# Optimization experiments

Hardware: AMD Instinct MI355X
Metric: run time of the kernel (lower is better)

## Reference

```python
import jax, jax.numpy as jnp
import numpy as np

N_NODES = 50000
N_EDGES = 400000
D = 128


def _rgg_layer(x, src, tgt, Wk, Wq, Wv, Ws, b, n_nodes):
    # Node-level projections (dense GEMMs, as in PyG which applies Linear before message passing)
    k = x @ Wk  # lin_key, gathered at targets
    q = x @ Wq  # lin_query, gathered at sources
    v = x @ Wv  # lin_value, gathered at sources
    # Per-edge gather + sigmoid gate + elementwise message
    eta = jax.nn.sigmoid(k[tgt] + q[src])  # [E, D]
    msg = eta * v[src]                      # [E, D]
    # Scatter-add aggregation to target nodes
    agg = jax.ops.segment_sum(msg, tgt, num_segments=n_nodes)
    # Root/skip connection + bias
    return agg + x @ Ws + b


def setup_inputs() -> dict:
    key = jax.random.key(0)
    ks = jax.random.split(key, 12)
    s = 1.0 / np.sqrt(D)
    x = jax.random.normal(ks[0], (N_NODES, D), dtype=jnp.float32)
    edge_index = jax.random.randint(ks[1], (2, N_EDGES), 0, N_NODES, dtype=jnp.int64)
    W = lambda k: (jax.random.normal(k, (D, D), dtype=jnp.float32) * s)
    return {
        "x": x,
        "edge_index": edge_index,
        "Wk1": W(ks[2]), "Wq1": W(ks[3]), "Wv1": W(ks[4]), "Ws1": W(ks[5]),
        "b1": jnp.zeros((D,), dtype=jnp.float32),
        "Wk2": W(ks[6]), "Wq2": W(ks[7]), "Wv2": W(ks[8]), "Ws2": W(ks[9]),
        "b2": jnp.zeros((D,), dtype=jnp.float32),
    }


def reference(x, edge_index, Wk1, Wq1, Wv1, Ws1, b1, Wk2, Wq2, Wv2, Ws2, b2):
    src, tgt = edge_index[0], edge_index[1]
    n = x.shape[0]
    h = _rgg_layer(x, src, tgt, Wk1, Wq1, Wv1, Ws1, b1, n)
    h = jax.nn.relu(h)
    # F.dropout treated as identity (deterministic/inference reference)
    out = _rgg_layer(h, src, tgt, Wk2, Wq2, Wv2, Ws2, b2, n)
    return out
```

## Files before the change

### kernel.cpp

```cpp
#include <hip/hip_runtime.h>

#define N_NODES 50000
#define D 128
#define N_EDGES 400000
#define NCHUNKS ((N_NODES + 255) / 256)
#define NBLK64 ((N_NODES + 63) / 64)
#define W_FRAG_SHORTS 16384

#define CVT_BLOCKS 3125
#define MW_BLOCKS  64
#define HIST_BLOCKS ((N_EDGES + 255) / 256)
#define PREP_BLOCKS (CVT_BLOCKS + MW_BLOCKS + HIST_BLOCKS)

typedef short s8v  __attribute__((ext_vector_type(8)));
typedef float f4v  __attribute__((ext_vector_type(4)));

__device__ __forceinline__ unsigned int f2bf(float f) {
    unsigned int u = __float_as_uint(f);
    u += 0x7FFFu + ((u >> 16) & 1u);
    return u >> 16;
}
__device__ __forceinline__ unsigned int packbf(float a, float b) {
    return (f2bf(b) << 16) | f2bf(a);
}
__device__ __forceinline__ float bflo(unsigned int u) { return __uint_as_float(u << 16); }
__device__ __forceinline__ float bfhi(unsigned int u) { return __uint_as_float(u & 0xFFFF0000u); }
__device__ __forceinline__ float sigm(float x) {
    return __builtin_amdgcn_rcpf(1.f + __expf(-x));
}

__global__ __launch_bounds__(256)
void prep_all(const float* __restrict__ X, short* __restrict__ Xb,
              const float* __restrict__ W0, const float* __restrict__ W1,
              const float* __restrict__ W2, const float* __restrict__ W3,
              const float* __restrict__ W4, const float* __restrict__ W5,
              const float* __restrict__ W6, const float* __restrict__ W7,
              short* __restrict__ Wt,
              const int* __restrict__ tgt, int* __restrict__ counts)
{
    const int b = blockIdx.x;
    if (b < CVT_BLOCKS) {
        const size_t i = ((size_t)b * 256 + threadIdx.x) * 8;
        float4 a0 = *(const float4*)(X + i);
        float4 a1 = *(const float4*)(X + i + 4);
        s8v v;
        v[0] = (short)f2bf(a0.x); v[1] = (short)f2bf(a0.y);
        v[2] = (short)f2bf(a0.z); v[3] = (short)f2bf(a0.w);
        v[4] = (short)f2bf(a1.x); v[5] = (short)f2bf(a1.y);
        v[6] = (short)f2bf(a1.z); v[7] = (short)f2bf(a1.w);
        *(s8v*)(Xb + i) = v;
    } else if (b < CVT_BLOCKS + MW_BLOCKS) {
        const int bb   = b - CVT_BLOCKS;
        const int wsel = bb >> 3;
        const float* W = (wsel == 0) ? W0 : (wsel == 1) ? W1 : (wsel == 2) ? W2 :
                         (wsel == 3) ? W3 : (wsel == 4) ? W4 : (wsel == 5) ? W5 :
                         (wsel == 6) ? W6 : W7;
        const int slot = (bb & 7) * 256 + threadIdx.x;
        const int frag = slot >> 6;
        const int lane = slot & 63;
        const int n    = (frag >> 2) * 16 + (lane & 15);
        const int kc   = frag & 3;
        const int quad = lane >> 4;
        const int k0   = kc * 32 + quad * 8;
        s8v v;
#pragma unroll
        for (int j = 0; j < 8; ++j)
            v[j] = (short)f2bf(W[(size_t)(k0 + j) * D + n]);
        *(s8v*)(Wt + (size_t)wsel * W_FRAG_SHORTS + (size_t)slot * 8) = v;
    } else {
        const int e = (b - CVT_BLOCKS - MW_BLOCKS) * 256 + threadIdx.x;
        if (e < N_EDGES) atomicAdd(&counts[tgt[e]], 1);
    }
}

__global__ __launch_bounds__(256)
void csr_scan(const int* __restrict__ counts, int* __restrict__ off,
              int* __restrict__ cursor, int* __restrict__ done_ctr,
              int* __restrict__ chunk_sum)
{
    __shared__ int s[256];
    const int b = blockIdx.x, t = threadIdx.x;
    const int i = b * 256 + t;
    const int v = (i < N_NODES) ? counts[i] : 0;
    s[t] = v;
    __syncthreads();
    for (int d = 1; d < 256; d <<= 1) {
        int tt = (t >= d) ? s[t - d] : 0;
        __syncthreads();
        s[t] += tt;
        __syncthreads();
    }
    const int incl = s[t];

    if (t == 255) {
        __hip_atomic_store(&chunk_sum[b], incl, __ATOMIC_RELAXED, __HIP_MEMORY_SCOPE_AGENT);
        __hip_atomic_fetch_add(done_ctr, 1, __ATOMIC_RELEASE, __HIP_MEMORY_SCOPE_AGENT);
    }
    if (t == 0) {
        while (__hip_atomic_load(done_ctr, __ATOMIC_ACQUIRE, __HIP_MEMORY_SCOPE_AGENT) < NCHUNKS)
            __builtin_amdgcn_s_sleep(8);
    }
    __syncthreads();

    const int pv = (t < b) ? __hip_atomic_load(&chunk_sum[t], __ATOMIC_RELAXED,
                                               __HIP_MEMORY_SCOPE_AGENT) : 0;
    __syncthreads();
    s[t] = pv;
    __syncthreads();
    for (int d = 128; d > 0; d >>= 1) {
        if (t < d) s[t] += s[t + d];
        __syncthreads();
    }
    const int base = s[0];

    if (i < N_NODES) {
        const int excl = base + incl - v;
        off[i]    = excl;
        cursor[i] = excl;
    }
    if (b == 0 && t == 0) off[N_NODES] = N_EDGES;
}

__device__ __forceinline__
void gemm_tile(int m0, const short* __restrict__ Xb, const short* __restrict__ WtL,
               const float* __restrict__ bias, short* __restrict__ Kb,
               unsigned int* __restrict__ QV, float* __restrict__ Agg,
               short* As, short* Bs, float* biasS)
{
    const int tid  = threadIdx.x;
    const int lane = tid & 63;
    const int w    = tid >> 6;
    const int wr   = w & 1;
    const int wc   = w >> 1;

    if (tid < 128) biasS[tid] = bias[tid];

#pragma unroll
    for (int i = 0; i < 4; ++i) {
        const int m   = (tid >> 4) + 16 * i;
        const int oct = tid & 15;
        const int row = m0 + m;
        s8v v = (s8v){0, 0, 0, 0, 0, 0, 0, 0};
        if (row < N_NODES) v = *(const s8v*)(Xb + (size_t)row * D + oct * 8);
        const int kc = oct >> 2, quad = oct & 3;
        const int frag = (m >> 4) * 4 + kc;
        const int slot = ((m & 15) + 16 * quad) ^ (kc << 1);
        *(s8v*)&As[frag * 512 + slot * 8] = v;
    }

    float* Cs = (float*)Bs;

    for (int sel = 0; sel < 4; ++sel) {
        __syncthreads();

        const short* Wf = WtL + (size_t)sel * W_FRAG_SHORTS;
#pragma unroll
        for (int j = 0; j < 8; ++j) {
            const int chunk = tid + 256 * j;
            __builtin_amdgcn_global_load_lds(
                (const __attribute__((address_space(1))) unsigned int*)(Wf + chunk * 8),
                (__attribute__((address_space(3))) unsigned int*)(&Bs[(chunk & ~63) * 8]),
                16, 0, 0);
        }
        __syncthreads();

        f4v acc[2][4];
#pragma unroll
        for (int mt = 0; mt < 2; ++mt)
#pragma unroll
            for (int nt = 0; nt < 4; ++nt)
                acc[mt][nt] = (f4v){0.f, 0.f, 0.f, 0.f};

#pragma unroll
        for (int kc = 0; kc < 4; ++kc) {
            const int sl = (lane ^ (kc << 1)) * 8;
            s8v a0 = *(const s8v*)&As[((2 * wr + 0) * 4 + kc) * 512 + sl];
            s8v a1 = *(const s8v*)&As[((2 * wr + 1) * 4 + kc) * 512 + sl];
#pragma unroll
            for (int nt = 0; nt < 4; ++nt) {
                s8v b = *(const s8v*)&Bs[((4 * wc + nt) * 4 + kc) * 512 + lane * 8];
                acc[0][nt] = __builtin_amdgcn_mfma_f32_16x16x32_bf16(a0, b, acc[0][nt], 0, 0, 0);
                acc[1][nt] = __builtin_amdgcn_mfma_f32_16x16x32_bf16(a1, b, acc[1][nt], 0, 0, 0);
            }
        }
        __syncthreads();

#pragma unroll
        for (int mt = 0; mt < 2; ++mt) {
            const int r0 = wr * 32 + mt * 16 + (lane >> 4) * 4;
#pragma unroll
            for (int nt = 0; nt < 4; ++nt) {
                const int col = wc * 64 + nt * 16 + (lane & 15);
                const int g = col >> 2, jj = col & 3;
#pragma unroll
                for (int i = 0; i < 4; ++i) {
                    const int row = r0 + i;
                    const int gs  = g ^ (((row >> 2) & 3) << 2);
                    Cs[row * 128 + gs * 4 + jj] = acc[mt][nt][i];
                }
            }
        }
        __syncthreads();

#pragma unroll
        for (int j = 0; j < 8; ++j) {
            const int c    = tid + 256 * j;
            const int row  = c >> 5;
            const int gg   = c & 31;
            const int gs   = gg ^ (((row >> 2) & 3) << 2);
            const f4v vv   = *(const f4v*)&Cs[row * 128 + gs * 4];
            const int grow = m0 + row;
            if (grow >= N_NODES) continue;
            if (sel == 3) {
                const float4 bv = *(const float4*)&biasS[gg * 4];
                float4 o = make_float4(vv[0] + bv.x, vv[1] + bv.y,
                                       vv[2] + bv.z, vv[3] + bv.w);
                *(float4*)&Agg[(size_t)grow * D + gg * 4] = o;
            } else {
                const unsigned int p0 = packbf(vv[0], vv[1]);
                const unsigned int p1 = packbf(vv[2], vv[3]);
                if (sel == 0) {
                    uint2* kp = (uint2*)((unsigned int*)Kb + (size_t)grow * 64 + gg * 2);
                    *kp = make_uint2(p0, p1);
                } else {
                    unsigned int* rowp = QV + (size_t)grow * 128 + gg * 4 + (sel == 2 ? 1 : 0);
                    rowp[0] = p0; rowp[2] = p1;
                }
            }
        }
    }
}

__global__ __launch_bounds__(256)
void gemm1_scatter(const short* __restrict__ Xb, const short* __restrict__ WtL,
                   const float* __restrict__ bias,
                   short* __restrict__ Kb, unsigned int* __restrict__ QV,
                   float* __restrict__ Agg,
                   const int* __restrict__ src, const int* __restrict__ tgt,
                   int* __restrict__ cursor, int* __restrict__ es)
{
    __shared__ __align__(16) short As[8192];
    __shared__ __align__(16) short Bs[16384];
    __shared__ __align__(16) float biasS[128];

    if (blockIdx.x < NBLK64) {
        gemm_tile(blockIdx.x * 64, Xb, WtL, bias, Kb, QV, Agg, As, Bs, biasS);
    } else {
        const int e = (blockIdx.x - NBLK64) * 256 + threadIdx.x;
        if (e < N_EDGES) {
            int pos = atomicAdd(&cursor[tgt[e]], 1);
            es[pos] = src[e];
        }
    }
}

__global__ __launch_bounds__(256)
void gemm_all(const short* __restrict__ Xb, const short* __restrict__ WtL,
              const float* __restrict__ bias,
              short* __restrict__ Kb, unsigned int* __restrict__ QV,
              float* __restrict__ Agg)
{
    __shared__ __align__(16) short As[8192];
    __shared__ __align__(16) short Bs[16384];
    __shared__ __align__(16) float biasS[128];
    gemm_tile(blockIdx.x * 64, Xb, WtL, bias, Kb, QV, Agg, As, Bs, biasS);
}

template<bool FIRST>
__global__ __launch_bounds__(256)
void node_agg(const int* __restrict__ off, const int* __restrict__ es,
              const short* __restrict__ K, const unsigned int* __restrict__ QV,
              const float* __restrict__ Skip, float* __restrict__ OutF,
              unsigned int* __restrict__ Hb)
{
    const int lane = threadIdx.x & 63;
    const int t    = __builtin_amdgcn_readfirstlane(blockIdx.x * 4 + (threadIdx.x >> 6));

    const unsigned int ku = ((const unsigned int*)K)[(size_t)t * 64 + lane];
    const float kx = bflo(ku), ky = bfhi(ku);
    const float2 sk = ((const float2*)Skip)[(size_t)t * 64 + lane];

    float ax = 0.f, ay = 0.f, bx = 0.f, by = 0.f;
    float cx = 0.f, cy = 0.f, dx = 0.f, dy = 0.f;
    const int e0 = __builtin_amdgcn_readfirstlane(off[t]);
    const int e1 = __builtin_amdgcn_readfirstlane(off[t + 1]);

    int e = e0;
    for (; e + 4 <= e1; e += 4) {
        const int s0 = __builtin_amdgcn_readfirstlane(es[e]);
        const int s1 = __builtin_amdgcn_readfirstlane(es[e + 1]);
        const int s2 = __builtin_amdgcn_readfirstlane(es[e + 2]);
        const int s3 = __builtin_amdgcn_readfirstlane(es[e + 3]);
        const uint2 qv0 = ((const uint2*)(QV + (size_t)s0 * 128))[lane];
        const uint2 qv1 = ((const uint2*)(QV + (size_t)s1 * 128))[lane];
        const uint2 qv2 = ((const uint2*)(QV + (size_t)s2 * 128))[lane];
        const uint2 qv3 = ((const uint2*)(QV + (size_t)s3 * 128))[lane];
        ax += bflo(qv0.y) * sigm(kx + bflo(qv0.x));
        ay += bfhi(qv0.y) * sigm(ky + bfhi(qv0.x));
        bx += bflo(qv1.y) * sigm(kx + bflo(qv1.x));
        by += bfhi(qv1.y) * sigm(ky + bfhi(qv1.x));
        cx += bflo(qv2.y) * sigm(kx + bflo(qv2.x));
        cy += bfhi(qv2.y) * sigm(ky + bfhi(qv2.x));
        dx += bflo(qv3.y) * sigm(kx + bflo(qv3.x));
        dy += bfhi(qv3.y) * sigm(ky + bfhi(qv3.x));
    }
    for (; e < e1; ++e) {
        const int s0 = __builtin_amdgcn_readfirstlane(es[e]);
        const uint2 qv0 = ((const uint2*)(QV + (size_t)s0 * 128))[lane];
        ax += bflo(qv0.y) * sigm(kx + bflo(qv0.x));
        ay += bfhi(qv0.y) * sigm(ky + bfhi(qv0.x));
    }

    const float rx = sk.x + (ax + bx) + (cx + dx);
    const float ry = sk.y + (ay + by) + (cy + dy);

    if (FIRST) {
        Hb[(size_t)t * 64 + lane] = packbf(fmaxf(rx, 0.f), fmaxf(ry, 0.f));
    } else {
        ((float2*)OutF)[(size_t)t * 64 + lane] = make_float2(rx, ry);
    }
}

extern "C" void kernel_launch(void* const* d_in, const int* in_sizes, int n_in,
                              void* d_out, int out_size, void* d_ws, size_t ws_size,
                              hipStream_t stream)
{
    const float* x   = (const float*)d_in[0];
    const int*   ei  = (const int*)d_in[1];
    const float* Wk1 = (const float*)d_in[2];
    const float* Wq1 = (const float*)d_in[3];
    const float* Wv1 = (const float*)d_in[4];
    const float* Ws1 = (const float*)d_in[5];
    const float* b1  = (const float*)d_in[6];
    const float* Wk2 = (const float*)d_in[7];
    const float* Wq2 = (const float*)d_in[8];
    const float* Wv2 = (const float*)d_in[9];
    const float* Ws2 = (const float*)d_in[10];
    const float* b2  = (const float*)d_in[11];

    const int* src = ei;
    const int* tgt = ei + N_EDGES;

    const size_t nd = (size_t)N_NODES * D;
    short* kb   = (short*)d_ws;
    short* qv   = kb + nd;
    short* xb   = qv + 2 * nd;
    short* hb   = xb + nd;
    float* agg1 = (float*)(hb + nd);
    short* wt   = (short*)(agg1 + nd);
    int* counts    = (int*)(wt + 8 * W_FRAG_SHORTS);
    int* done_ctr  = counts + N_NODES;
    int* off       = counts + N_NODES + 2;
    int* cursor    = off + N_NODES + 1;
    int* es        = cursor + N_NODES;
    int* chunk_sum = es + N_EDGES;
    float* out = (float*)d_out;

    hipMemsetAsync(counts, 0, (N_NODES + 2) * sizeof(int), stream);
    prep_all<<<PREP_BLOCKS, 256, 0, stream>>>(x, xb,
                                              Wk1, Wq1, Wv1, Ws1, Wk2, Wq2, Wv2, Ws2,
                                              wt, tgt, counts);
    csr_scan<<<NCHUNKS, 256, 0, stream>>>(counts, off, cursor, done_ctr, chunk_sum);

    gemm1_scatter<<<NBLK64 + HIST_BLOCKS, 256, 0, stream>>>(
        xb, wt, b1, kb, (unsigned int*)qv, agg1, src, tgt, cursor, es);
    node_agg<true><<<N_NODES / 4, 256, 0, stream>>>(off, es, kb, (const unsigned int*)qv,
                                                    agg1, nullptr, (unsigned int*)hb);

    gemm_all<<<NBLK64, 256, 0, stream>>>(hb, wt + 4 * W_FRAG_SHORTS, b2,
                                         kb, (unsigned int*)qv, out);
    node_agg<false><<<N_NODES / 4, 256, 0, stream>>>(off, es, kb, (const unsigned int*)qv,
                                                     out, out, nullptr);
}
```

Before: 269.2 us.

## Fuse x bf16 conversion into GEMM, store skip in bf16, batch edge index loads

The separate fp32-to-bf16 conversion pass over x is removed, and the first GEMM tile now reads fp32 x and converts it while staging into LDS. The layer-1 skip/bias result is stored as bf16 instead of fp32, which halves that buffer's traffic at some cost in precision. Q and V are computed back to back so each row is written with a single 16-byte store instead of strided 4-byte stores. The aggregation loop now loads 8 edge indices with one vector load and broadcasts them via readlane, which cuts scalar load latency per edge.

```diff
diff --git a/kernel.cpp b/kernel.cpp
--- a/kernel.cpp
+++ b/kernel.cpp
@@ -7,10 +7,9 @@
 #define NBLK64 ((N_NODES + 63) / 64)
 #define W_FRAG_SHORTS 16384
 
-#define CVT_BLOCKS 3125
 #define MW_BLOCKS  64
 #define HIST_BLOCKS ((N_EDGES + 255) / 256)
-#define PREP_BLOCKS (CVT_BLOCKS + MW_BLOCKS + HIST_BLOCKS)
+#define PREP_BLOCKS (MW_BLOCKS + HIST_BLOCKS)
 
 typedef short s8v  __attribute__((ext_vector_type(8)));
 typedef float f4v  __attribute__((ext_vector_type(4)));
@@ -30,8 +29,7 @@
 }
 
 __global__ __launch_bounds__(256)
-void prep_all(const float* __restrict__ X, short* __restrict__ Xb,
-              const float* __restrict__ W0, const float* __restrict__ W1,
+void prep_all(const float* __restrict__ W0, const float* __restrict__ W1,
               const float* __restrict__ W2, const float* __restrict__ W3,
               const float* __restrict__ W4, const float* __restrict__ W5,
               const float* __restrict__ W6, const float* __restrict__ W7,
@@ -39,23 +37,12 @@
               const int* __restrict__ tgt, int* __restrict__ counts)
 {
     const int b = blockIdx.x;
-    if (b < CVT_BLOCKS) {
-        const size_t i = ((size_t)b * 256 + threadIdx.x) * 8;
-        float4 a0 = *(const float4*)(X + i);
-        float4 a1 = *(const float4*)(X + i + 4);
-        s8v v;
-        v[0] = (short)f2bf(a0.x); v[1] = (short)f2bf(a0.y);
-        v[2] = (short)f2bf(a0.z); v[3] = (short)f2bf(a0.w);
-        v[4] = (short)f2bf(a1.x); v[5] = (short)f2bf(a1.y);
-        v[6] = (short)f2bf(a1.z); v[7] = (short)f2bf(a1.w);
-        *(s8v*)(Xb + i) = v;
-    } else if (b < CVT_BLOCKS + MW_BLOCKS) {
-        const int bb   = b - CVT_BLOCKS;
-        const int wsel = bb >> 3;
+    if (b < MW_BLOCKS) {
+        const int wsel = b >> 3;
         const float* W = (wsel == 0) ? W0 : (wsel == 1) ? W1 : (wsel == 2) ? W2 :
                          (wsel == 3) ? W3 : (wsel == 4) ? W4 : (wsel == 5) ? W5 :
                          (wsel == 6) ? W6 : W7;
-        const int slot = (bb & 7) * 256 + threadIdx.x;
+        const int slot = (b & 7) * 256 + threadIdx.x;
         const int frag = slot >> 6;
         const int lane = slot & 63;
         const int n    = (frag >> 2) * 16 + (lane & 15);
@@ -68,7 +55,7 @@
             v[j] = (short)f2bf(W[(size_t)(k0 + j) * D + n]);
         *(s8v*)(Wt + (size_t)wsel * W_FRAG_SHORTS + (size_t)slot * 8) = v;
     } else {
-        const int e = (b - CVT_BLOCKS - MW_BLOCKS) * 256 + threadIdx.x;
+        const int e = (b - MW_BLOCKS) * 256 + threadIdx.x;
         if (e < N_EDGES) atomicAdd(&counts[tgt[e]], 1);
     }
 }
@@ -122,9 +109,67 @@
 }
 
 __device__ __forceinline__
-void gemm_tile(int m0, const short* __restrict__ Xb, const short* __restrict__ WtL,
-               const float* __restrict__ bias, short* __restrict__ Kb,
-               unsigned int* __restrict__ QV, float* __restrict__ Agg,
+void stage_b(const short* __restrict__ Wf, short* Bs, int tid)
+{
+#pragma unroll
+    for (int j = 0; j < 8; ++j) {
+        const int chunk = tid + 256 * j;
+        __builtin_amdgcn_global_load_lds(
+            (const __attribute__((address_space(1))) unsigned int*)(Wf + chunk * 8),
+            (__attribute__((address_space(3))) unsigned int*)(&Bs[(chunk & ~63) * 8]),
+            16, 0, 0);
+    }
+}
+
+__device__ __forceinline__
+void mfma_phase(const short* As, const short* Bs, int lane, int wr, int wc,
+                f4v acc[2][4])
+{
+#pragma unroll
+    for (int mt = 0; mt < 2; ++mt)
+#pragma unroll
+        for (int nt = 0; nt < 4; ++nt)
+            acc[mt][nt] = (f4v){0.f, 0.f, 0.f, 0.f};
+#pragma unroll
+    for (int kc = 0; kc < 4; ++kc) {
+        const int sl = (lane ^ (kc << 1)) * 8;
+        s8v a0 = *(const s8v*)&As[((2 * wr + 0) * 4 + kc) * 512 + sl];
+        s8v a1 = *(const s8v*)&As[((2 * wr + 1) * 4 + kc) * 512 + sl];
+#pragma unroll
+        for (int nt = 0; nt < 4; ++nt) {
+            s8v b = *(const s8v*)&Bs[((4 * wc + nt) * 4 + kc) * 512 + lane * 8];
+            acc[0][nt] = __builtin_amdgcn_mfma_f32_16x16x32_bf16(a0, b, acc[0][nt], 0, 0, 0);
+            acc[1][nt] = __builtin_amdgcn_mfma_f32_16x16x32_bf16(a1, b, acc[1][nt], 0, 0, 0);
+        }
+    }
+}
+
+__device__ __forceinline__
+void c_to_lds(float* Cs, int lane, int wr, int wc, const f4v acc[2][4])
+{
+#pragma unroll
+    for (int mt = 0; mt < 2; ++mt) {
+        const int r0 = wr * 32 + mt * 16 + (lane >> 4) * 4;
+#pragma unroll
+        for (int nt = 0; nt < 4; ++nt) {
+            const int col = wc * 64 + nt * 16 + (lane & 15);
+            const int g = col >> 2, jj = col & 3;
+#pragma unroll
+            for (int i = 0; i < 4; ++i) {
+                const int row = r0 + i;
+                const int gs  = g ^ (((row >> 2) & 3) << 2);
+                Cs[row * 128 + gs * 4 + jj] = acc[mt][nt][i];
+            }
+        }
+    }
+}
+
+template<bool X_FP32, bool AGG_BF16>
+__device__ __forceinline__
+void gemm_tile(int m0, const float* __restrict__ Xf, const short* __restrict__ Xb,
+               const short* __restrict__ WtL, const float* __restrict__ bias,
+               short* __restrict__ Kb, unsigned int* __restrict__ QV,
+               float* __restrict__ AggF, unsigned int* __restrict__ AggB,
                short* As, short* Bs, float* biasS)
 {
     const int tid  = threadIdx.x;
@@ -141,7 +186,19 @@
         const int oct = tid & 15;
         const int row = m0 + m;
         s8v v = (s8v){0, 0, 0, 0, 0, 0, 0, 0};
-        if (row < N_NODES) v = *(const s8v*)(Xb + (size_t)row * D + oct * 8);
+        if (row < N_NODES) {
+            if (X_FP32) {
+                const float* p = Xf + (size_t)row * D + oct * 8;
+                float4 a0 = *(const float4*)p;
+                float4 a1 = *(const float4*)(p + 4);
+                v[0] = (short)f2bf(a0.x); v[1] = (short)f2bf(a0.y);
+                v[2] = (short)f2bf(a0.z); v[3] = (short)f2bf(a0.w);
+                v[4] = (short)f2bf(a1.x); v[5] = (short)f2bf(a1.y);
+                v[6] = (short)f2bf(a1.z); v[7] = (short)f2bf(a1.w);
+            } else {
+                v = *(const s8v*)(Xb + (size_t)row * D + oct * 8);
+            }
+        }
         const int kc = oct >> 2, quad = oct & 3;
         const int frag = (m >> 4) * 4 + kc;
         const int slot = ((m & 15) + 16 * quad) ^ (kc << 1);
@@ -149,93 +206,99 @@
     }
 
     float* Cs = (float*)Bs;
-
-    for (int sel = 0; sel < 4; ++sel) {
-        __syncthreads();
-
-        const short* Wf = WtL + (size_t)sel * W_FRAG_SHORTS;
-#pragma unroll
-        for (int j = 0; j < 8; ++j) {
-            const int chunk = tid + 256 * j;
-            __builtin_amdgcn_global_load_lds(
-                (const __attribute__((address_space(1))) unsigned int*)(Wf + chunk * 8),
-                (__attribute__((address_space(3))) unsigned int*)(&Bs[(chunk & ~63) * 8]),
-                16, 0, 0);
-        }
-        __syncthreads();
-
-        f4v acc[2][4];
-#pragma unroll
-        for (int mt = 0; mt < 2; ++mt)
-#pragma unroll
-            for (int nt = 0; nt < 4; ++nt)
-                acc[mt][nt] = (f4v){0.f, 0.f, 0.f, 0.f};
-
-#pragma unroll
-        for (int kc = 0; kc < 4; ++kc) {
-            const int sl = (lane ^ (kc << 1)) * 8;
-            s8v a0 = *(const s8v*)&As[((2 * wr + 0) * 4 + kc) * 512 + sl];
-            s8v a1 = *(const s8v*)&As[((2 * wr + 1) * 4 + kc) * 512 + sl];
-#pragma unroll
-            for (int nt = 0; nt < 4; ++nt) {
-                s8v b = *(const s8v*)&Bs[((4 * wc + nt) * 4 + kc) * 512 + lane * 8];
-                acc[0][nt] = __builtin_amdgcn_mfma_f32_16x16x32_bf16(a0, b, acc[0][nt], 0, 0, 0);
-                acc[1][nt] = __builtin_amdgcn_mfma_f32_16x16x32_bf16(a1, b, acc[1][nt], 0, 0, 0);
-            }
-        }
-        __syncthreads();
-
-#pragma unroll
-        for (int mt = 0; mt < 2; ++mt) {
-            const int r0 = wr * 32 + mt * 16 + (lane >> 4) * 4;
-#pragma unroll
-            for (int nt = 0; nt < 4; ++nt) {
-                const int col = wc * 64 + nt * 16 + (lane & 15);
-                const int g = col >> 2, jj = col & 3;
-#pragma unroll
-                for (int i = 0; i < 4; ++i) {
-                    const int row = r0 + i;
-                    const int gs  = g ^ (((row >> 2) & 3) << 2);
-                    Cs[row * 128 + gs * 4 + jj] = acc[mt][nt][i];
-                }
-            }
-        }
-        __syncthreads();
-
-#pragma unroll
-        for (int j = 0; j < 8; ++j) {
-            const int c    = tid + 256 * j;
-            const int row  = c >> 5;
-            const int gg   = c & 31;
-            const int gs   = gg ^ (((row >> 2) & 3) << 2);
-            const f4v vv   = *(const f4v*)&Cs[row * 128 + gs * 4];
-            const int grow = m0 + row;
-            if (grow >= N_NODES) continue;
-            if (sel == 3) {
-                const float4 bv = *(const float4*)&biasS[gg * 4];
-                float4 o = make_float4(vv[0] + bv.x, vv[1] + bv.y,
-                                       vv[2] + bv.z, vv[3] + bv.w);
-                *(float4*)&Agg[(size_t)grow * D + gg * 4] = o;
-            } else {
-                const unsigned int p0 = packbf(vv[0], vv[1]);
-                const unsigned int p1 = packbf(vv[2], vv[3]);
-                if (sel == 0) {
-                    uint2* kp = (uint2*)((unsigned int*)Kb + (size_t)grow * 64 + gg * 2);
-                    *kp = make_uint2(p0, p1);
-                } else {
-                    unsigned int* rowp = QV + (size_t)grow * 128 + gg * 4 + (sel == 2 ? 1 : 0);
-                    rowp[0] = p0; rowp[2] = p1;
-                }
-            }
+    f4v acc[2][4];
+
+    __syncthreads();
+    stage_b(WtL + 0 * W_FRAG_SHORTS, Bs, tid);
+    __syncthreads();
+    mfma_phase(As, Bs, lane, wr, wc, acc);
+    __syncthreads();
+    c_to_lds(Cs, lane, wr, wc, acc);
+    __syncthreads();
+#pragma unroll
+    for (int j = 0; j < 8; ++j) {
+        const int c   = tid + 256 * j;
+        const int row = c >> 5, gg = c & 31;
+        const int gs  = gg ^ (((row >> 2) & 3) << 2);
+        const f4v vv  = *(const f4v*)&Cs[row * 128 + gs * 4];
+        const int grow = m0 + row;
+        if (grow < N_NODES) {
+            uint2* kp = (uint2*)((unsigned int*)Kb + (size_t)grow * 64 + gg * 2);
+            *kp = make_uint2(packbf(vv[0], vv[1]), packbf(vv[2], vv[3]));
+        }
+    }
+
+    f4v accV[2][4];
+    __syncthreads();
+    stage_b(WtL + 1 * W_FRAG_SHORTS, Bs, tid);
+    __syncthreads();
+    mfma_phase(As, Bs, lane, wr, wc, acc);
+    __syncthreads();
+    stage_b(WtL + 2 * W_FRAG_SHORTS, Bs, tid);
+    __syncthreads();
+    mfma_phase(As, Bs, lane, wr, wc, accV);
+    __syncthreads();
+    c_to_lds(Cs, lane, wr, wc, acc);
+    __syncthreads();
+    unsigned int qp0[8], qp1[8];
+#pragma unroll
+    for (int j = 0; j < 8; ++j) {
+        const int c   = tid + 256 * j;
+        const int row = c >> 5, gg = c & 31;
+        const int gs  = gg ^ (((row >> 2) & 3) << 2);
+        const f4v vv  = *(const f4v*)&Cs[row * 128 + gs * 4];
+        qp0[j] = packbf(vv[0], vv[1]);
+        qp1[j] = packbf(vv[2], vv[3]);
+    }
+    __syncthreads();
+    c_to_lds(Cs, lane, wr, wc, accV);
+    __syncthreads();
+#pragma unroll
+    for (int j = 0; j < 8; ++j) {
+        const int c   = tid + 256 * j;
+        const int row = c >> 5, gg = c & 31;
+        const int gs  = gg ^ (((row >> 2) & 3) << 2);
+        const f4v vv  = *(const f4v*)&Cs[row * 128 + gs * 4];
+        const int grow = m0 + row;
+        if (grow < N_NODES) {
+            uint4* qvp = (uint4*)(QV + (size_t)grow * 128 + gg * 4);
+            *qvp = make_uint4(qp0[j], packbf(vv[0], vv[1]),
+                              qp1[j], packbf(vv[2], vv[3]));
+        }
+    }
+
+    __syncthreads();
+    stage_b(WtL + 3 * W_FRAG_SHORTS, Bs, tid);
+    __syncthreads();
+    mfma_phase(As, Bs, lane, wr, wc, acc);
+    __syncthreads();
+    c_to_lds(Cs, lane, wr, wc, acc);
+    __syncthreads();
+#pragma unroll
+    for (int j = 0; j < 8; ++j) {
+        const int c   = tid + 256 * j;
+        const int row = c >> 5, gg = c & 31;
+        const int gs  = gg ^ (((row >> 2) & 3) << 2);
+        const f4v vv  = *(const f4v*)&Cs[row * 128 + gs * 4];
+        const int grow = m0 + row;
+        if (grow >= N_NODES) continue;
+        const float4 bv = *(const float4*)&biasS[gg * 4];
+        const float o0 = vv[0] + bv.x, o1 = vv[1] + bv.y;
+        const float o2 = vv[2] + bv.z, o3 = vv[3] + bv.w;
+        if (AGG_BF16) {
+            uint2* ap = (uint2*)(AggB + (size_t)grow * 64 + gg * 2);
+            *ap = make_uint2(packbf(o0, o1), packbf(o2, o3));
+        } else {
+            *(float4*)&AggF[(size_t)grow * D + gg * 4] = make_float4(o0, o1, o2, o3);
         }
     }
 }
 
 __global__ __launch_bounds__(256)
-void gemm1_scatter(const short* __restrict__ Xb, const short* __restrict__ WtL,
+void gemm1_scatter(const float* __restrict__ X, const short* __restrict__ WtL,
                    const float* __restrict__ bias,
                    short* __restrict__ Kb, unsigned int* __restrict__ QV,
-                   float* __restrict__ Agg,
+                   unsigned int* __restrict__ AggB,
                    const int* __restrict__ src, const int* __restrict__ tgt,
                    int* __restrict__ cursor, int* __restrict__ es)
 {
@@ -244,7 +307,8 @@
     __shared__ __align__(16) float biasS[128];
 
     if (blockIdx.x < NBLK64) {
-        gemm_tile(blockIdx.x * 64, Xb, WtL, bias, Kb, QV, Agg, As, Bs, biasS);
+        gemm_tile<true, true>(blockIdx.x * 64, X, nullptr, WtL, bias,
+                              Kb, QV, nullptr, AggB, As, Bs, biasS);
     } else {
         const int e = (blockIdx.x - NBLK64) * 256 + threadIdx.x;
         if (e < N_EDGES) {
@@ -255,22 +319,23 @@
 }
 
 __global__ __launch_bounds__(256)
-void gemm_all(const short* __restrict__ Xb, const short* __restrict__ WtL,
-              const float* __restrict__ bias,
-              short* __restrict__ Kb, unsigned int* __restrict__ QV,
-              float* __restrict__ Agg)
+void gemm2(const short* __restrict__ Hb, const short* __restrict__ WtL,
+           const float* __restrict__ bias,
+           short* __restrict__ Kb, unsigned int* __restrict__ QV,
+           float* __restrict__ AggF)
 {
     __shared__ __align__(16) short As[8192];
     __shared__ __align__(16) short Bs[16384];
     __shared__ __align__(16) float biasS[128];
-    gemm_tile(blockIdx.x * 64, Xb, WtL, bias, Kb, QV, Agg, As, Bs, biasS);
+    gemm_tile<false, false>(blockIdx.x * 64, nullptr, Hb, WtL, bias,
+                            Kb, QV, AggF, nullptr, As, Bs, biasS);
 }
 
 template<bool FIRST>
 __global__ __launch_bounds__(256)
 void node_agg(const int* __restrict__ off, const int* __restrict__ es,
               const short* __restrict__ K, const unsigned int* __restrict__ QV,
-              const float* __restrict__ Skip, float* __restrict__ OutF,
+              const void* __restrict__ Skip, float* __restrict__ OutF,
               unsigned int* __restrict__ Hb)
 {
     const int lane = threadIdx.x & 63;
@@ -278,41 +343,69 @@
 
     const unsigned int ku = ((const unsigned int*)K)[(size_t)t * 64 + lane];
     const float kx = bflo(ku), ky = bfhi(ku);
-    const float2 sk = ((const float2*)Skip)[(size_t)t * 64 + lane];
+
+    float skx, sky;
+    if (FIRST) {
+        const unsigned int su = ((const unsigned int*)Skip)[(size_t)t * 64 + lane];
+        skx = bflo(su); sky = bfhi(su);
+    } else {
+        const float2 s2 = ((const float2*)Skip)[(size_t)t * 64 + lane];
+        skx = s2.x; sky = s2.y;
+    }
 
     float ax = 0.f, ay = 0.f, bx = 0.f, by = 0.f;
-    float cx = 0.f, cy = 0.f, dx = 0.f, dy = 0.f;
     const int e0 = __builtin_amdgcn_readfirstlane(off[t]);
     const int e1 = __builtin_amdgcn_readfirstlane(off[t + 1]);
 
     int e = e0;
-    for (; e + 4 <= e1; e += 4) {
-        const int s0 = __builtin_amdgcn_readfirstlane(es[e]);
-        const int s1 = __builtin_amdgcn_readfirstlane(es[e + 1]);
-        const int s2 = __builtin_amdgcn_readfirstlane(es[e + 2]);
-        const int s3 = __builtin_amdgcn_readfirstlane(es[e + 3]);
-        const uint2 qv0 = ((const uint2*)(QV + (size_t)s0 * 128))[lane];
-        const uint2 qv1 = ((const uint2*)(QV + (size_t)s1 * 128))[lane];
-        const uint2 qv2 = ((const uint2*)(QV + (size_t)s2 * 128))[lane];
-        const uint2 qv3 = ((const uint2*)(QV + (size_t)s3 * 128))[lane];
-        ax += bflo(qv0.y) * sigm(kx + bflo(qv0.x));
-        ay += bfhi(qv0.y) * sigm(ky + bfhi(qv0.x));
-        bx += bflo(qv1.y) * sigm(kx + bflo(qv1.x));
-        by += bfhi(qv1.y) * sigm(ky + bfhi(qv1.x));
-        cx += bflo(qv2.y) * sigm(kx + bflo(qv2.x));
-        cy += bfhi(qv2.y) * sigm(ky + bfhi(qv2.x));
-        dx += bflo(qv3.y) * sigm(kx + bflo(qv3.x));
-        dy += bfhi(qv3.y) * sigm(ky + bfhi(qv3.x));
+    for (; e + 8 <= e1; e += 8) {
+        const int sv = es[e + (lane & 7)];
+        uint2 g[8];
+#pragma unroll
+        for (int u = 0; u < 8; ++u) {
+            const int s = __builtin_amdgcn_readlane(sv, u);
+            g[u] = ((const uint2*)(QV + (size_t)s * 128))[lane];
+        }
+#pragma unroll
+        for (int u = 0; u < 8; ++u) {
+            if (u & 1) {
+                bx += bflo(g[u].y) * sigm(kx + bflo(g[u].x));
+                by += bfhi(g[u].y) * sigm(ky + bfhi(g[u].x));
+            } else {
+                ax += bflo(g[u].y) * sigm(kx + bflo(g[u].x));
+                ay += bfhi(g[u].y) * sigm(ky + bfhi(g[u].x));
+            }
+        }
+    }
+    if (e + 4 <= e1) {
+        const int sv = es[e + (lane & 3)];
+        uint2 g[4];
+#pragma unroll
+        for (int u = 0; u < 4; ++u) {
+            const int s = __builtin_amdgcn_readlane(sv, u);
+            g[u] = ((const uint2*)(QV + (size_t)s * 128))[lane];
+        }
+#pragma unroll
+        for (int u = 0; u < 4; ++u) {
+            if (u & 1) {
+                bx += bflo(g[u].y) * sigm(kx + bflo(g[u].x));
+                by += bfhi(g[u].y) * sigm(ky + bfhi(g[u].x));
+            } else {
+                ax += bflo(g[u].y) * sigm(kx + bflo(g[u].x));
+                ay += bfhi(g[u].y) * sigm(ky + bfhi(g[u].x));
+            }
+        }
+        e += 4;
     }
     for (; e < e1; ++e) {
         const int s0 = __builtin_amdgcn_readfirstlane(es[e]);
-        const uint2 qv0 = ((const uint2*)(QV + (size_t)s0 * 128))[lane];
-        ax += bflo(qv0.y) * sigm(kx + bflo(qv0.x));
-        ay += bfhi(qv0.y) * sigm(ky + bfhi(qv0.x));
-    }
-
-    const float rx = sk.x + (ax + bx) + (cx + dx);
-    const float ry = sk.y + (ay + by) + (cy + dy);
+        const uint2 g0 = ((const uint2*)(QV + (size_t)s0 * 128))[lane];
+        ax += bflo(g0.y) * sigm(kx + bflo(g0.x));
+        ay += bfhi(g0.y) * sigm(ky + bfhi(g0.x));
+    }
+
+    const float rx = skx + ax + bx;
+    const float ry = sky + ay + by;
 
     if (FIRST) {
         Hb[(size_t)t * 64 + lane] = packbf(fmaxf(rx, 0.f), fmaxf(ry, 0.f));
@@ -344,10 +437,9 @@
     const size_t nd = (size_t)N_NODES * D;
     short* kb   = (short*)d_ws;
     short* qv   = kb + nd;
-    short* xb   = qv + 2 * nd;
-    short* hb   = xb + nd;
-    float* agg1 = (float*)(hb + nd);
-    short* wt   = (short*)(agg1 + nd);
+    short* hb   = qv + 2 * nd;
+    short* ag1  = hb + nd;
+    short* wt   = ag1 + nd;
     int* counts    = (int*)(wt + 8 * W_FRAG_SHORTS);
     int* done_ctr  = counts + N_NODES;
     int* off       = counts + N_NODES + 2;
@@ -357,18 +449,17 @@
     float* out = (float*)d_out;
 
     hipMemsetAsync(counts, 0, (N_NODES + 2) * sizeof(int), stream);
-    prep_all<<<PREP_BLOCKS, 256, 0, stream>>>(x, xb,
-                                              Wk1, Wq1, Wv1, Ws1, Wk2, Wq2, Wv2, Ws2,
+    prep_all<<<PREP_BLOCKS, 256, 0, stream>>>(Wk1, Wq1, Wv1, Ws1, Wk2, Wq2, Wv2, Ws2,
                                               wt, tgt, counts);
     csr_scan<<<NCHUNKS, 256, 0, stream>>>(counts, off, cursor, done_ctr, chunk_sum);
 
     gemm1_scatter<<<NBLK64 + HIST_BLOCKS, 256, 0, stream>>>(
-        xb, wt, b1, kb, (unsigned int*)qv, agg1, src, tgt, cursor, es);
+        x, wt, b1, kb, (unsigned int*)qv, (unsigned int*)ag1, src, tgt, cursor, es);
     node_agg<true><<<N_NODES / 4, 256, 0, stream>>>(off, es, kb, (const unsigned int*)qv,
-                                                    agg1, nullptr, (unsigned int*)hb);
-
-    gemm_all<<<NBLK64, 256, 0, stream>>>(hb, wt + 4 * W_FRAG_SHORTS, b2,
-                                         kb, (unsigned int*)qv, out);
+                                                    ag1, nullptr, (unsigned int*)hb);
+
+    gemm2<<<NBLK64, 256, 0, stream>>>(hb, wt + 4 * W_FRAG_SHORTS, b2,
+                                      kb, (unsigned int*)qv, out);
     node_agg<false><<<N_NODES / 4, 256, 0, stream>>>(off, es, kb, (const unsigned int*)qv,
                                                      out, out, nullptr);
 }
```

Result: faster. 263.0 us (-2.3%).
